# Kernel tuning notes

Measured on AMD Instinct MI355X. Metric: run time of the kernel, lower is better.

Reference implementation:

```python
import jax, jax.numpy as jnp
import numpy as np

B, LMAX, M, D, V = 32768, 24, 10, 300, 36  # batch, max word len, max_length, embedding_dim, vocab


def setup_inputs() -> dict:
    key = jax.random.key(0)
    k1, k2, k3, k4 = jax.random.split(key, 4)
    lengths = jax.random.randint(k2, (B,), 1, LMAX + 1)  # word lengths in [1, LMAX]
    tokens = jax.random.randint(k1, (B, LMAX), 0, V)
    # zero out slots past each word's length (they are never read with nonzero weight)
    tokens = jnp.where(jnp.arange(LMAX)[None, :] < lengths[:, None], tokens, 0)
    emb_table = jax.random.normal(k3, (V, D), dtype=jnp.float32)
    pad_table = jax.random.normal(k4, (1, D), dtype=jnp.float32)
    return {"emb_table": emb_table, "pad_table": pad_table,
            "tokens": tokens, "lengths": lengths}


def reference(emb_table, pad_table, tokens, lengths):
    # Per-word char embedding lookup: [B, LMAX, D]
    embs = emb_table[tokens]

    # ---- interpolate branch (words with L >= M): bilinear, align_corners=True.
    # Output width == input width (D) so width interp is identity; only the
    # character axis is linearly resampled: src = i * (L-1) / (M-1).
    Lf = lengths.astype(jnp.float32)[:, None]                      # [B,1]
    pos = jnp.arange(M, dtype=jnp.float32)[None, :] * (Lf - 1.0) / (M - 1)  # [B,M]
    lo = jnp.floor(pos).astype(jnp.int32)                          # [B,M]
    hi = jnp.minimum(lo + 1, lengths[:, None].astype(jnp.int32) - 1)
    w = (pos - lo.astype(jnp.float32))[..., None]                  # [B,M,1]
    g_lo = jnp.take_along_axis(embs, lo[..., None], axis=1)        # [B,M,D]
    g_hi = jnp.take_along_axis(embs, hi[..., None], axis=1)        # [B,M,D]
    interp = g_lo * (1.0 - w) + g_hi * w

    # ---- padding branch (words with L < M): first L rows are embeddings,
    # remaining rows are the learned padding embedding.
    pad_vec = pad_table[0]                                         # [D]
    valid = jnp.arange(M)[None, :, None] < lengths[:, None, None]  # [B,M,1]
    padded = jnp.where(valid, embs[:, :M, :], pad_vec)

    out = jnp.where((lengths < M)[:, None, None], padded, interp)  # [B,M,D]
    return out
```

## Files before the change

### kernel.cpp

```cpp
#include <hip/hip_runtime.h>

#define BATCH 32768
#define LMAX  24
#define MOUT  10
#define DIM   300
#define VOCAB 36
#define D4    (DIM / 4)
#define NROW  (BATCH * MOUT)
#define N4    (NROW * D4)
#define PAD_OFF (VOCAB * DIM)
#define LDSF  (VOCAB * DIM + DIM)

#define TPB   512
#define NBLK  750
#define NTHR  (TPB * NBLK)
#define ITERS (N4 / NTHR)

__device__ __forceinline__ void row_desc(const int* __restrict__ tokens,
                                         const int* __restrict__ lengths,
                                         int r, int& lo_off, int& hi_off, float& w)
{
    const int b = r / MOUT;
    const int i = r - b * MOUT;
    const int L = lengths[b];
    const int* trow = tokens + b * LMAX;
    if (L < MOUT) {
        const int off = (i < L) ? trow[i] * DIM : PAD_OFF;
        lo_off = off; hi_off = off; w = 0.0f;
    } else {
        const float pos = ((float)i * (float)(L - 1)) / (float)(MOUT - 1);
        const int   lo  = (int)floorf(pos);
        const int   hi  = min(lo + 1, L - 1);
        w = pos - (float)lo;
        lo_off = trow[lo] * DIM;
        hi_off = trow[hi] * DIM;
    }
}

__global__ __launch_bounds__(TPB) void emb_fused_kernel(
    const float* __restrict__ emb,
    const float* __restrict__ pad,
    const int*   __restrict__ tokens,
    const int*   __restrict__ lengths,
    float4*      __restrict__ out)
{
    __shared__ float lds[LDSF];
    {
        const float4* e4 = (const float4*)emb;
        float4* l4 = (float4*)lds;
        for (int i = threadIdx.x; i < VOCAB * D4; i += TPB) l4[i] = e4[i];
        const float4* p4 = (const float4*)pad;
        for (int i = threadIdx.x; i < D4; i += TPB) l4[VOCAB * D4 + i] = p4[i];
    }
    __syncthreads();

    const int tid = blockIdx.x * TPB + threadIdx.x;
    const int stride = NTHR;

    int e = tid;
    for (int it = 0; it < ITERS / 4; ++it) {
        const int e0 = e, e1 = e + stride, e2 = e + 2 * stride, e3 = e + 3 * stride;

        const int r0 = e0 / D4, r1 = e1 / D4, r2 = e2 / D4, r3 = e3 / D4;
        const int j0 = e0 - r0 * D4, j1 = e1 - r1 * D4, j2 = e2 - r2 * D4, j3 = e3 - r3 * D4;

        int lo0, hi0, lo1, hi1, lo2, hi2, lo3, hi3;
        float w0, w1, w2, w3;
        row_desc(tokens, lengths, r0, lo0, hi0, w0);
        row_desc(tokens, lengths, r1, lo1, hi1, w1);
        row_desc(tokens, lengths, r2, lo2, hi2, w2);
        row_desc(tokens, lengths, r3, lo3, hi3, w3);

        const float4 a0 = *(const float4*)&lds[lo0 + 4 * j0];
        const float4 b0 = *(const float4*)&lds[hi0 + 4 * j0];
        const float4 a1 = *(const float4*)&lds[lo1 + 4 * j1];
        const float4 b1 = *(const float4*)&lds[hi1 + 4 * j1];
        const float4 a2 = *(const float4*)&lds[lo2 + 4 * j2];
        const float4 b2 = *(const float4*)&lds[hi2 + 4 * j2];
        const float4 a3 = *(const float4*)&lds[lo3 + 4 * j3];
        const float4 b3 = *(const float4*)&lds[hi3 + 4 * j3];

        const float u0 = 1.0f - w0;
        const float u1 = 1.0f - w1;
        const float u2 = 1.0f - w2;
        const float u3 = 1.0f - w3;

        float4 v0, v1, v2, v3;
        v0.x = a0.x * u0 + b0.x * w0; v0.y = a0.y * u0 + b0.y * w0;
        v0.z = a0.z * u0 + b0.z * w0; v0.w = a0.w * u0 + b0.w * w0;
        v1.x = a1.x * u1 + b1.x * w1; v1.y = a1.y * u1 + b1.y * w1;
        v1.z = a1.z * u1 + b1.z * w1; v1.w = a1.w * u1 + b1.w * w1;
        v2.x = a2.x * u2 + b2.x * w2; v2.y = a2.y * u2 + b2.y * w2;
        v2.z = a2.z * u2 + b2.z * w2; v2.w = a2.w * u2 + b2.w * w2;
        v3.x = a3.x * u3 + b3.x * w3; v3.y = a3.y * u3 + b3.y * w3;
        v3.z = a3.z * u3 + b3.z * w3; v3.w = a3.w * u3 + b3.w * w3;

        out[e0] = v0;
        out[e1] = v1;
        out[e2] = v2;
        out[e3] = v3;

        e += 4 * stride;
    }
}

extern "C" void kernel_launch(void* const* d_in, const int* in_sizes, int n_in,
                              void* d_out, int out_size, void* d_ws, size_t ws_size,
                              hipStream_t stream) {
    const float* emb     = (const float*)d_in[0];
    const float* pad     = (const float*)d_in[1];
    const int*   tokens  = (const int*)d_in[2];
    const int*   lengths = (const int*)d_in[3];
    float4* out = (float4*)d_out;

    (void)d_ws; (void)ws_size;

    emb_fused_kernel<<<NBLK, TPB, 0, stream>>>(emb, pad, tokens, lengths, out);
}
```

Before: 446.0 us.

## Precompute per-row descriptors in LDS with contiguous block ranges and nontemporal stores

Each block now owns a contiguous range of output elements instead of a grid-strided one. Before the main loop it computes one descriptor per output row (lo/hi table offsets and the interpolation weight) into shared memory. The main loop then reads the descriptor from LDS instead of re-running the per-element global loads of lengths and tokens and the float division. Output writes switch to nontemporal stores to reduce cache pollution. The cost is an extra LDS array and a prologue phase before the barrier.

```diff
diff --git a/kernel.cpp b/kernel.cpp
--- a/kernel.cpp
+++ b/kernel.cpp
@@ -9,83 +9,89 @@
 #define NROW  (BATCH * MOUT)
 #define N4    (NROW * D4)
 #define PAD_OFF (VOCAB * DIM)
-#define LDSF  (VOCAB * DIM + DIM)
+#define TABF  (VOCAB * DIM + DIM)
+
+typedef float nfloat4 __attribute__((ext_vector_type(4)));
 
 #define TPB   512
 #define NBLK  750
-#define NTHR  (TPB * NBLK)
-#define ITERS (N4 / NTHR)
+#define EPB   (N4 / NBLK)
+#define ITERS (EPB / TPB)
+#define MAXD  440
 
-__device__ __forceinline__ void row_desc(const int* __restrict__ tokens,
-                                         const int* __restrict__ lengths,
-                                         int r, int& lo_off, int& hi_off, float& w)
-{
-    const int b = r / MOUT;
-    const int i = r - b * MOUT;
-    const int L = lengths[b];
-    const int* trow = tokens + b * LMAX;
-    if (L < MOUT) {
-        const int off = (i < L) ? trow[i] * DIM : PAD_OFF;
-        lo_off = off; hi_off = off; w = 0.0f;
-    } else {
-        const float pos = ((float)i * (float)(L - 1)) / (float)(MOUT - 1);
-        const int   lo  = (int)floorf(pos);
-        const int   hi  = min(lo + 1, L - 1);
-        w = pos - (float)lo;
-        lo_off = trow[lo] * DIM;
-        hi_off = trow[hi] * DIM;
-    }
-}
-
-__global__ __launch_bounds__(TPB) void emb_fused_kernel(
+__global__ __launch_bounds__(TPB) void emb_onepass_kernel(
     const float* __restrict__ emb,
     const float* __restrict__ pad,
     const int*   __restrict__ tokens,
     const int*   __restrict__ lengths,
-    float4*      __restrict__ out)
+    float*       __restrict__ out)
 {
-    __shared__ float lds[LDSF];
+    __shared__ float tab[TABF];
+    __shared__ int4  dsc[MAXD];
+
     {
         const float4* e4 = (const float4*)emb;
-        float4* l4 = (float4*)lds;
-        for (int i = threadIdx.x; i < VOCAB * D4; i += TPB) l4[i] = e4[i];
+        float4* t4 = (float4*)tab;
+        for (int i = threadIdx.x; i < VOCAB * D4; i += TPB) t4[i] = e4[i];
         const float4* p4 = (const float4*)pad;
-        for (int i = threadIdx.x; i < D4; i += TPB) l4[VOCAB * D4 + i] = p4[i];
+        for (int i = threadIdx.x; i < D4; i += TPB) t4[VOCAB * D4 + i] = p4[i];
+    }
+
+    const int eBase = blockIdx.x * EPB;
+    const int rBase = eBase / D4;
+    const int rEnd  = (eBase + EPB - 1) / D4;
+    const int nR    = rEnd - rBase + 1;
+    for (int idx = threadIdx.x; idx < nR; idx += TPB) {
+        const int r = rBase + idx;
+        const int b = r / MOUT;
+        const int i = r - b * MOUT;
+        const int L = lengths[b];
+        int lo_off, hi_off;
+        float w;
+        if (L < MOUT) {
+            const int off = (i < L) ? tokens[b * LMAX + i] * DIM : PAD_OFF;
+            lo_off = off; hi_off = off; w = 0.0f;
+        } else {
+            const float pos = ((float)i * (float)(L - 1)) / (float)(MOUT - 1);
+            const int   lo  = (int)floorf(pos);
+            const int   hi  = min(lo + 1, L - 1);
+            w = pos - (float)lo;
+            lo_off = tokens[b * LMAX + lo] * DIM;
+            hi_off = tokens[b * LMAX + hi] * DIM;
+        }
+        dsc[idx] = make_int4(lo_off, hi_off, __float_as_int(w), 0);
     }
     __syncthreads();
 
-    const int tid = blockIdx.x * TPB + threadIdx.x;
-    const int stride = NTHR;
-
-    int e = tid;
-    for (int it = 0; it < ITERS / 4; ++it) {
-        const int e0 = e, e1 = e + stride, e2 = e + 2 * stride, e3 = e + 3 * stride;
+    nfloat4* out4 = (nfloat4*)out;
+    int e = eBase + threadIdx.x;
+    for (int g = 0; g < ITERS / 4; ++g) {
+        const int e0 = e, e1 = e + TPB, e2 = e + 2 * TPB, e3 = e + 3 * TPB;
 
         const int r0 = e0 / D4, r1 = e1 / D4, r2 = e2 / D4, r3 = e3 / D4;
-        const int j0 = e0 - r0 * D4, j1 = e1 - r1 * D4, j2 = e2 - r2 * D4, j3 = e3 - r3 * D4;
+        const int j0 = e0 - r0 * D4, j1 = e1 - r1 * D4;
+        const int j2 = e2 - r2 * D4, j3 = e3 - r3 * D4;
 
-        int lo0, hi0, lo1, hi1, lo2, hi2, lo3, hi3;
-        float w0, w1, w2, w3;
-        row_desc(tokens, lengths, r0, lo0, hi0, w0);
-        row_desc(tokens, lengths, r1, lo1, hi1, w1);
-        row_desc(tokens, lengths, r2, lo2, hi2, w2);
-        row_desc(tokens, lengths, r3, lo3, hi3, w3);
+        const int4 d0 = dsc[r0 - rBase];
+        const int4 d1 = dsc[r1 - rBase];
+        const int4 d2 = dsc[r2 - rBase];
+        const int4 d3 = dsc[r3 - rBase];
 
-        const float4 a0 = *(const float4*)&lds[lo0 + 4 * j0];
-        const float4 b0 = *(const float4*)&lds[hi0 + 4 * j0];
-        const float4 a1 = *(const float4*)&lds[lo1 + 4 * j1];
-        const float4 b1 = *(const float4*)&lds[hi1 + 4 * j1];
-        const float4 a2 = *(const float4*)&lds[lo2 + 4 * j2];
-        const float4 b2 = *(const float4*)&lds[hi2 + 4 * j2];
-        const float4 a3 = *(const float4*)&lds[lo3 + 4 * j3];
-        const float4 b3 = *(const float4*)&lds[hi3 + 4 * j3];
+        const float4 a0 = *(const float4*)&tab[d0.x + 4 * j0];
+        const float4 b0 = *(const float4*)&tab[d0.y + 4 * j0];
+        const float4 a1 = *(const float4*)&tab[d1.x + 4 * j1];
+        const float4 b1 = *(const float4*)&tab[d1.y + 4 * j1];
+        const float4 a2 = *(const float4*)&tab[d2.x + 4 * j2];
+        const float4 b2 = *(const float4*)&tab[d2.y + 4 * j2];
+        const float4 a3 = *(const float4*)&tab[d3.x + 4 * j3];
+        const float4 b3 = *(const float4*)&tab[d3.y + 4 * j3];
 
-        const float u0 = 1.0f - w0;
-        const float u1 = 1.0f - w1;
-        const float u2 = 1.0f - w2;
-        const float u3 = 1.0f - w3;
+        const float w0 = __int_as_float(d0.z), u0 = 1.0f - w0;
+        const float w1 = __int_as_float(d1.z), u1 = 1.0f - w1;
+        const float w2 = __int_as_float(d2.z), u2 = 1.0f - w2;
+        const float w3 = __int_as_float(d3.z), u3 = 1.0f - w3;
 
-        float4 v0, v1, v2, v3;
+        nfloat4 v0, v1, v2, v3;
         v0.x = a0.x * u0 + b0.x * w0; v0.y = a0.y * u0 + b0.y * w0;
         v0.z = a0.z * u0 + b0.z * w0; v0.w = a0.w * u0 + b0.w * w0;
         v1.x = a1.x * u1 + b1.x * w1; v1.y = a1.y * u1 + b1.y * w1;
@@ -95,12 +101,12 @@
         v3.x = a3.x * u3 + b3.x * w3; v3.y = a3.y * u3 + b3.y * w3;
         v3.z = a3.z * u3 + b3.z * w3; v3.w = a3.w * u3 + b3.w * w3;
 
-        out[e0] = v0;
-        out[e1] = v1;
-        out[e2] = v2;
-        out[e3] = v3;
+        __builtin_nontemporal_store(v0, out4 + e0);
+        __builtin_nontemporal_store(v1, out4 + e1);
+        __builtin_nontemporal_store(v2, out4 + e2);
+        __builtin_nontemporal_store(v3, out4 + e3);
 
-        e += 4 * stride;
+        e += 4 * TPB;
     }
 }
 
@@ -111,9 +117,9 @@
     const float* pad     = (const float*)d_in[1];
     const int*   tokens  = (const int*)d_in[2];
     const int*   lengths = (const int*)d_in[3];
-    float4* out = (float4*)d_out;
+    float* out = (float*)d_out;
 
     (void)d_ws; (void)ws_size;
 
-    emb_fused_kernel<<<NBLK, TPB, 0, stream>>>(emb, pad, tokens, lengths, out);
+    emb_onepass_kernel<<<NBLK, TPB, 0, stream>>>(emb, pad, tokens, lengths, out);
 }
```

Measured after the change: 399.3 us. 1.12x faster.
